# Performance work log

Hardware: AMD Instinct MI355X
Metric: run time of the kernel (lower is better)

## Reference

```python
import jax, jax.numpy as jnp
import numpy as np

B, DIM, HEADS, HD, H, W = 1, 256, 8, 32, 64, 64
MLP = int(DIM * 4.0)
EPS = 1e-5


def _ln(x, g, b):
    # LayerNorm over channel dim of NCHW (torch applies it on NHWC last dim)
    mu = x.mean(axis=1, keepdims=True)
    var = ((x - mu) ** 2).mean(axis=1, keepdims=True)
    return (x - mu) / jnp.sqrt(var + EPS) * g[None, :, None, None] + b[None, :, None, None]


def _c1(x, w, b):
    # 1x1 conv: w is [out, in]
    return jnp.einsum('bchw,oc->bohw', x, w) + b[None, :, None, None]


def _c3(x, w, b):
    y = jax.lax.conv_general_dilated(x, w, (1, 1), ((1, 1), (1, 1)),
                                     dimension_numbers=('NCHW', 'OIHW', 'NCHW'))
    return y + b[None, :, None, None]


def setup_inputs() -> dict:
    key = jax.random.key(0)
    ks = jax.random.split(key, 16)
    init = lambda k, s: jax.random.normal(k, s, jnp.float32) * 0.02
    d = {}
    d['rgb_feat'] = jax.random.normal(ks[0], (B, DIM, H, W), jnp.float32)
    d['dpt_feat'] = jax.random.normal(ks[1], (B, DIM, H, W), jnp.float32)
    d['x_dpt'] = jax.random.normal(ks[2], (B, 1, 1024, 1024), jnp.float32)
    d['wq'] = init(ks[3], (DIM, DIM)); d['bq'] = jnp.zeros((DIM,), jnp.float32)
    d['wk'] = init(ks[4], (DIM, DIM)); d['bk'] = jnp.zeros((DIM,), jnp.float32)
    d['wv'] = init(ks[5], (DIM, DIM)); d['bv'] = jnp.zeros((DIM,), jnp.float32)
    d['wo'] = init(ks[6], (DIM, DIM)); d['bo'] = jnp.zeros((DIM,), jnp.float32)
    d['g_rgb'] = jnp.ones((DIM,), jnp.float32); d['b_rgb'] = jnp.zeros((DIM,), jnp.float32)
    d['g_dpt'] = jnp.ones((DIM,), jnp.float32); d['b_dpt'] = jnp.zeros((DIM,), jnp.float32)
    d['g1'] = jnp.ones((DIM,), jnp.float32); d['b1'] = jnp.zeros((DIM,), jnp.float32)
    d['g2'] = jnp.ones((DIM,), jnp.float32); d['b2'] = jnp.zeros((DIM,), jnp.float32)
    d['w_mlp1'] = init(ks[7], (MLP, DIM)); d['b_mlp1'] = jnp.zeros((MLP,), jnp.float32)
    d['w_mlp2'] = init(ks[8], (DIM, MLP)); d['b_mlp2'] = jnp.zeros((DIM,), jnp.float32)
    d['w_de1'] = init(ks[9], (DIM, 1, 3, 3)); d['b_de1'] = jnp.zeros((DIM,), jnp.float32)
    d['w_de2'] = init(ks[10], (DIM, DIM)); d['b_de2'] = jnp.zeros((DIM,), jnp.float32)
    d['pos_emb'] = init(ks[11], (1, DIM, 1, 1))
    d['scale'] = jnp.sqrt(jnp.float32(HD))
    return d


def reference(rgb_feat, dpt_feat, x_dpt, wq, bq, wk, bk, wv, bv, wo, bo,
              g_rgb, b_rgb, g_dpt, b_dpt, g1, b1, g2, b2,
              w_mlp1, b_mlp1, w_mlp2, b_mlp2, w_de1, b_de1, w_de2, b_de2,
              pos_emb, scale):
    Bn, C, Hh, Ww = rgb_feat.shape
    n = Hh * Ww
    rgb_ln = _ln(rgb_feat, g_rgb, b_rgb)
    dpt_ln = _ln(dpt_feat, g_dpt, b_dpt)
    # depth positional embedding: bilinear downsample (align_corners=False) + conv3x3 + relu + conv1x1
    xd = jax.image.resize(x_dpt, (Bn, 1, Hh, Ww), method='bilinear', antialias=False)
    pe = _c1(jax.nn.relu(_c3(xd, w_de1, b_de1)), w_de2, b_de2)
    rgb_ln = rgb_ln + pos_emb + pe
    dpt_ln = dpt_ln + pos_emb + pe
    # QKV as [B, heads, head_dim, N]
    q = _c1(rgb_ln, wq, bq).reshape(Bn, HEADS, HD, n)
    k = _c1(dpt_ln, wk, bk).reshape(Bn, HEADS, HD, n)
    v = _c1(dpt_ln, wv, bv).reshape(Bn, HEADS, HD, n)
    scores = jnp.einsum('bhdn,bhdm->bhnm', q, k) / scale
    attn = jax.nn.softmax(scores, axis=-1)  # dropout is identity in eval
    fused = jnp.einsum('bhnm,bhdm->bhdn', attn, v).reshape(Bn, C, Hh, Ww)
    out = _c1(fused, wo, bo) + rgb_feat
    out_ln = _ln(out, g1, b1)
    h = jax.nn.gelu(_c1(out_ln, w_mlp1, b_mlp1), approximate=False)
    mlp_out = _c1(h, w_mlp2, b_mlp2)
    out2 = mlp_out + out_ln
    return _ln(out2, g2, b2)
```

## Files before the change

kernel.cpp:

```cpp
#include <hip/hip_runtime.h>
#include <hip/hip_bf16.h>
#include <math.h>

constexpr int NTOK = 4096;
constexpr int CDIM = 256;
constexpr int MLPD = 1024;
constexpr int SPLIT = 4;
constexpr float EPS_LN = 1e-5f;

typedef __attribute__((ext_vector_type(8))) short bf16x8;
typedef __attribute__((ext_vector_type(4))) float floatx4;
typedef unsigned short u16;
typedef unsigned int u32;

__device__ __forceinline__ u16 f2bf(float x) {
    union { float f; u32 u; } v; v.f = x;
    u32 r = v.u + 0x7fff + ((v.u >> 16) & 1);
    return (u16)(r >> 16);
}
__device__ __forceinline__ float bf2f(u16 u) {
    union { u32 i; float f; } v; v.i = ((u32)u) << 16; return v.f;
}
__device__ __forceinline__ u32 pkbf(float a, float b) {
    __hip_bfloat162 h = __float22bfloat162_rn(make_float2(a, b));
    union { __hip_bfloat162 h; u32 u; } v; v.h = h; return v.u;
}
__device__ __forceinline__ float gelu_exact(float x) {
    return 0.5f * x * (1.0f + erff(x * 0.70710678118654752f));
}

__global__ __launch_bounds__(256) void k_tr2(const float* __restrict__ in0,
                                             float* __restrict__ out0,
                                             const float* __restrict__ in1,
                                             float* __restrict__ out1, int R, int C) {
    const float* in = blockIdx.z ? in1 : in0;
    float* out = blockIdx.z ? out1 : out0;
    __shared__ float T[64][65];
    int r0 = blockIdx.y * 64, c0 = blockIdx.x * 64;
    int t = threadIdx.x;
    int rr = t >> 4, cc = (t & 15) * 4;
#pragma unroll
    for (int i = 0; i < 4; ++i) {
        int row = i * 16 + rr;
        float4 v = *(const float4*)(in + (size_t)(r0 + row) * C + c0 + cc);
        T[row][cc] = v.x; T[row][cc + 1] = v.y; T[row][cc + 2] = v.z; T[row][cc + 3] = v.w;
    }
    __syncthreads();
#pragma unroll
    for (int i = 0; i < 4; ++i) {
        int a = i * 16 + rr;
        float4 v;
        v.x = T[cc][a]; v.y = T[cc + 1][a]; v.z = T[cc + 2][a]; v.w = T[cc + 3][a];
        *(float4*)(out + (size_t)(c0 + a) * R + r0 + cc) = v;
    }
}

__global__ __launch_bounds__(256) void k_prep(const float* __restrict__ xdpt,
                                              const float* __restrict__ w3,
                                              const float* __restrict__ b3,
                                              u16* __restrict__ y,
                                              const float* __restrict__ wq,
                                              const float* __restrict__ wk,
                                              const float* __restrict__ wv,
                                              const float* __restrict__ wo,
                                              const float* __restrict__ wde2,
                                              const float* __restrict__ wm1,
                                              const float* __restrict__ wm2,
                                              u16* __restrict__ arena) {
    int blk = blockIdx.x;
    int t = threadIdx.x;
    if (blk < 256) {
        __shared__ float nb[3][18];
        int n0 = blk * 16;
        int yy = n0 >> 6, x0 = n0 & 63;
        if (t < 54) {
            int r = t / 18, cc = t % 18;
            int sy = yy - 1 + r, sx = x0 - 1 + cc;
            float v = 0.f;
            if (sy >= 0 && sy < 64 && sx >= 0 && sx < 64) {
                int r0 = 16 * sy + 7, c0 = 16 * sx + 7;
                v = 0.25f * (xdpt[r0 * 1024 + c0] + xdpt[r0 * 1024 + c0 + 1] +
                             xdpt[(r0 + 1) * 1024 + c0] + xdpt[(r0 + 1) * 1024 + c0 + 1]);
            }
            nb[r][cc] = v;
        }
        __syncthreads();
        float wv9[9];
#pragma unroll
        for (int i = 0; i < 9; ++i) wv9[i] = w3[t * 9 + i];
        float bb = b3[t];
#pragma unroll
        for (int k = 0; k < 16; ++k) {
            float acc = bb;
#pragma unroll
            for (int r = 0; r < 3; ++r)
#pragma unroll
                for (int kx = 0; kx < 3; ++kx) acc += wv9[r * 3 + kx] * nb[r][k + kx];
            y[(size_t)(n0 + k) * CDIM + t] = f2bf(fmaxf(acc, 0.f));
        }
    } else {
        int e0 = (blk - 256) * 1024 + t * 4;
        const float* src; int off;
        if (e0 < 65536)       { src = wq;   off = 0; }
        else if (e0 < 131072) { src = wk;   off = 65536; }
        else if (e0 < 196608) { src = wv;   off = 131072; }
        else if (e0 < 262144) { src = wo;   off = 196608; }
        else if (e0 < 327680) { src = wde2; off = 262144; }
        else if (e0 < 589824) { src = wm1;  off = 327680; }
        else                  { src = wm2;  off = 589824; }
        float4 v = *(const float4*)(src + (e0 - off));
        uint2 o; o.x = pkbf(v.x, v.y); o.y = pkbf(v.z, v.w);
        *(uint2*)(arena + e0) = o;
    }
}

__global__ __launch_bounds__(256) void k_lnT(const void* __restrict__ xA,
                                             const float* __restrict__ gA,
                                             const float* __restrict__ bA,
                                             void* __restrict__ yA,
                                             const void* __restrict__ xB,
                                             const float* __restrict__ gB,
                                             const float* __restrict__ bB,
                                             void* __restrict__ yB,
                                             const u16* __restrict__ pe,
                                             const float* __restrict__ pos,
                                             int xf32, int yf32) {
    const void* x; const float* g; const float* bb; void* y;
    if (blockIdx.y == 0) { x = xA; g = gA; bb = bA; y = yA; }
    else                 { x = xB; g = gB; bb = bB; y = yB; }
    int n = blockIdx.x * 4 + (threadIdx.x >> 6);
    int lane = threadIdx.x & 63;
    int c = lane * 4;
    float4 xv;
    if (xf32) {
        xv = *((const float4*)x + (size_t)n * 64 + lane);
    } else {
        ushort4 u = *((const ushort4*)x + (size_t)n * 64 + lane);
        xv = make_float4(bf2f(u.x), bf2f(u.y), bf2f(u.z), bf2f(u.w));
    }
    float s = xv.x + xv.y + xv.z + xv.w;
    float s2 = xv.x * xv.x + xv.y * xv.y + xv.z * xv.z + xv.w * xv.w;
#pragma unroll
    for (int off = 1; off < 64; off <<= 1) {
        s += __shfl_xor(s, off, 64);
        s2 += __shfl_xor(s2, off, 64);
    }
    float mu = s * (1.0f / 256.0f);
    float var = s2 * (1.0f / 256.0f) - mu * mu;
    float rsd = rsqrtf(var + EPS_LN);
    float4 g4 = *(const float4*)(g + c);
    float4 b4 = *(const float4*)(bb + c);
    float4 o;
    o.x = (xv.x - mu) * rsd * g4.x + b4.x;
    o.y = (xv.y - mu) * rsd * g4.y + b4.y;
    o.z = (xv.z - mu) * rsd * g4.z + b4.z;
    o.w = (xv.w - mu) * rsd * g4.w + b4.w;
    if (pe) {
        float4 p4 = *(const float4*)(pos + c);
        ushort4 pu = *((const ushort4*)pe + (size_t)n * 64 + lane);
        o.x += p4.x + bf2f(pu.x);
        o.y += p4.y + bf2f(pu.y);
        o.z += p4.z + bf2f(pu.z);
        o.w += p4.w + bf2f(pu.w);
    }
    if (yf32) {
        *((float4*)y + (size_t)n * 64 + lane) = o;
    } else {
        ushort4 ou;
        ou.x = f2bf(o.x); ou.y = f2bf(o.y); ou.z = f2bf(o.z); ou.w = f2bf(o.w);
        *((ushort4*)y + (size_t)n * 64 + lane) = ou;
    }
}

#define LDB 72
__global__ __launch_bounds__(256) void k_bmm(const u16* __restrict__ X0, const void* __restrict__ W0,
                                             const float* __restrict__ B0, void* __restrict__ Y0, int f0,
                                             const u16* __restrict__ X1, const void* __restrict__ W1,
                                             const float* __restrict__ B1, void* __restrict__ Y1, int f1,
                                             const u16* __restrict__ X2, const void* __restrict__ W2,
                                             const float* __restrict__ B2, void* __restrict__ Y2, int f2,
                                             const void* __restrict__ res, const float* __restrict__ scl,
                                             int M, int K) {
    const u16* X; const void* Wp; const float* bias; void* Yp; int flags;
    if (blockIdx.z == 0)      { X = X0; Wp = W0; bias = B0; Yp = Y0; flags = f0; }
    else if (blockIdx.z == 1) { X = X1; Wp = W1; bias = B1; Yp = Y1; flags = f1; }
    else                      { X = X2; Wp = W2; bias = B2; Yp = Y2; flags = f2; }
    __shared__ u16 Xs[64 * LDB];
    __shared__ u16 Ws[64 * LDB];
    int tid = threadIdx.x;
    int wid = tid >> 6, lane = tid & 63;
    int lo16 = lane & 15, quad = lane >> 4;
    int wy = wid & 1, wx = wid >> 1;
    int n0 = blockIdx.x * 64, m0 = blockIdx.y * 64;
    int srow = tid >> 2, sseg = tid & 3;

    floatx4 acc[2][2];
#pragma unroll
    for (int i = 0; i < 2; ++i)
#pragma unroll
        for (int j = 0; j < 2; ++j) acc[i][j] = floatx4{0.f, 0.f, 0.f, 0.f};

    for (int k0 = 0; k0 < K; k0 += 64) {
        const u16* xp = X + (size_t)(n0 + srow) * K + k0 + sseg * 16;
        uint4 xr0 = *(const uint4*)xp;
        uint4 xr1 = *(const uint4*)(xp + 8);
        uint4 wb0, wb1;
        if (flags & 32) {
            const u16* wp = (const u16*)Wp + (size_t)(m0 + srow) * K + k0 + sseg * 16;
            wb0 = *(const uint4*)wp;
            wb1 = *(const uint4*)(wp + 8);
        } else {
            const float* wp = (const float*)Wp + (size_t)(m0 + srow) * K + k0 + sseg * 16;
            float4 w0 = *(const float4*)wp;
            float4 w1 = *(const float4*)(wp + 4);
            float4 w2 = *(const float4*)(wp + 8);
            float4 w3 = *(const float4*)(wp + 12);
            wb0.x = pkbf(w0.x, w0.y); wb0.y = pkbf(w0.z, w0.w);
            wb0.z = pkbf(w1.x, w1.y); wb0.w = pkbf(w1.z, w1.w);
            wb1.x = pkbf(w2.x, w2.y); wb1.y = pkbf(w2.z, w2.w);
            wb1.z = pkbf(w3.x, w3.y); wb1.w = pkbf(w3.z, w3.w);
        }
        if (k0) __syncthreads();
        *(uint4*)&Xs[srow * LDB + sseg * 16] = xr0;
        *(uint4*)&Xs[srow * LDB + sseg * 16 + 8] = xr1;
        *(uint4*)&Ws[srow * LDB + sseg * 16] = wb0;
        *(uint4*)&Ws[srow * LDB + sseg * 16 + 8] = wb1;
        __syncthreads();

        const u16* As = (flags & 2) ? Ws : Xs;
        const u16* Bs = (flags & 2) ? Xs : Ws;
#pragma unroll
        for (int h = 0; h < 2; ++h) {
            int ko = h * 32 + quad * 8;
            bf16x8 a0 = *(const bf16x8*)&As[(wy * 32 + lo16) * LDB + ko];
            bf16x8 a1 = *(const bf16x8*)&As[(wy * 32 + 16 + lo16) * LDB + ko];
            bf16x8 b0 = *(const bf16x8*)&Bs[(wx * 32 + lo16) * LDB + ko];
            bf16x8 b1 = *(const bf16x8*)&Bs[(wx * 32 + 16 + lo16) * LDB + ko];
            acc[0][0] = __builtin_amdgcn_mfma_f32_16x16x32_bf16(a0, b0, acc[0][0], 0, 0, 0);
            acc[0][1] = __builtin_amdgcn_mfma_f32_16x16x32_bf16(a0, b1, acc[0][1], 0, 0, 0);
            acc[1][0] = __builtin_amdgcn_mfma_f32_16x16x32_bf16(a1, b0, acc[1][0], 0, 0, 0);
            acc[1][1] = __builtin_amdgcn_mfma_f32_16x16x32_bf16(a1, b1, acc[1][1], 0, 0, 0);
        }
    }

    u16* Y = (u16*)Yp;
    if (flags & 2) {
#pragma unroll
        for (int i = 0; i < 2; ++i)
#pragma unroll
            for (int r = 0; r < 4; ++r) {
                int ch = m0 + wy * 32 + i * 16 + quad * 4 + r;
                float bb = bias[ch];
#pragma unroll
                for (int j = 0; j < 2; ++j) {
                    int tok = n0 + wx * 32 + j * 16 + lo16;
                    Y[(size_t)ch * NTOK + tok] = f2bf(acc[i][j][r] + bb);
                }
            }
    } else {
        float smul = (flags & 16) ? 1.4426950408889634f / scl[0] : 1.0f;
        float bj0 = bias[m0 + wx * 32 + lo16];
        float bj1 = bias[m0 + wx * 32 + 16 + lo16];
        const float* rf = (const float*)res;
        const u16* rb = (const u16*)res;
#pragma unroll
        for (int i = 0; i < 2; ++i)
#pragma unroll
            for (int j = 0; j < 2; ++j) {
                int ch = m0 + wx * 32 + j * 16 + lo16;
                float bb = j ? bj1 : bj0;
#pragma unroll
                for (int r = 0; r < 4; ++r) {
                    int tok = n0 + wy * 32 + i * 16 + quad * 4 + r;
                    float v = (acc[i][j][r] + bb) * smul;
                    if (flags & 1) v = gelu_exact(v);
                    if (flags & 4) v += rf[(size_t)tok * M + ch];
                    if (flags & 8) v += bf2f(rb[(size_t)tok * M + ch]);
                    if (flags & 64)
                        Y[((size_t)(ch >> 5) * NTOK + tok) * 32 + (ch & 31)] = f2bf(v);
                    else
                        Y[(size_t)tok * M + ch] = f2bf(v);
                }
            }
    }
}

#define LDK 40
#define LDV 72
__global__ __launch_bounds__(256, 8) void k_fattn(const u16* __restrict__ Qh,
                                                  const u16* __restrict__ Kh,
                                                  const u16* __restrict__ Vc,
                                                  u16* __restrict__ Op,
                                                  float* __restrict__ Lp) {
    int h = blockIdx.y;
    int q0 = blockIdx.x * 64;
    int sp = blockIdx.z;
    int tid = threadIdx.x;
    int wid = tid >> 6, lane = tid & 63;
    int lo16 = lane & 15, quad = lane >> 4;

    __shared__ u16 Kt[64 * LDK];
    __shared__ u16 Vt[32 * LDV];
    __shared__ u16 Pt[4][16 * LDV];

    bf16x8 aq = *(const bf16x8*)(Qh + ((size_t)h * NTOK + q0 + wid * 16 + lo16) * 32 + quad * 8);

    floatx4 o0 = {0.f, 0.f, 0.f, 0.f};
    floatx4 o1 = {0.f, 0.f, 0.f, 0.f};
    float l = 0.f;

    int krow = tid >> 2, kseg = tid & 3;
    int vrow = tid >> 3, vseg = tid & 7;
    int kbase = sp * (NTOK / SPLIT);

    for (int kt = 0; kt < NTOK / SPLIT / 64; ++kt) {
        int k0 = kbase + kt * 64;
        uint4 kreg = *(const uint4*)(Kh + ((size_t)h * NTOK + k0 + krow) * 32 + kseg * 8);
        uint4 vreg = *(const uint4*)(Vc + (size_t)(h * 32 + vrow) * NTOK + k0 + vseg * 8);
        __syncthreads();
        *(uint4*)&Kt[krow * LDK + kseg * 8] = kreg;
        *(uint4*)&Vt[vrow * LDV + vseg * 8] = vreg;
        __syncthreads();

        floatx4 s[4];
        floatx4 z = {0.f, 0.f, 0.f, 0.f};
#pragma unroll
        for (int c = 0; c < 4; ++c) {
            bf16x8 ak = *(const bf16x8*)&Kt[(c * 16 + lo16) * LDK + quad * 8];
            s[c] = __builtin_amdgcn_mfma_f32_16x16x32_bf16(ak, aq, z, 0, 0, 0);
        }
        float rs = 0.f;
#pragma unroll
        for (int c = 0; c < 4; ++c)
#pragma unroll
            for (int r = 0; r < 4; ++r) {
                float p = __builtin_amdgcn_exp2f(s[c][r]);
                s[c][r] = p;
                rs += p;
            }
        rs += __shfl_xor(rs, 16, 64);
        rs += __shfl_xor(rs, 32, 64);
        l += rs;
#pragma unroll
        for (int c = 0; c < 4; ++c) {
            uint2 w;
            w.x = pkbf(s[c][0], s[c][1]);
            w.y = pkbf(s[c][2], s[c][3]);
            *(uint2*)&Pt[wid][lo16 * LDV + c * 16 + quad * 4] = w;
        }
#pragma unroll
        for (int kc = 0; kc < 2; ++kc) {
            bf16x8 bp = *(const bf16x8*)&Pt[wid][lo16 * LDV + kc * 32 + quad * 8];
            bf16x8 av0 = *(const bf16x8*)&Vt[lo16 * LDV + kc * 32 + quad * 8];
            bf16x8 av1 = *(const bf16x8*)&Vt[(16 + lo16) * LDV + kc * 32 + quad * 8];
            o0 = __builtin_amdgcn_mfma_f32_16x16x32_bf16(av0, bp, o0, 0, 0, 0);
            o1 = __builtin_amdgcn_mfma_f32_16x16x32_bf16(av1, bp, o1, 0, 0, 0);
        }
    }

    size_t tok = q0 + wid * 16 + lo16;
    size_t obase = ((size_t)(sp * 8 + h) * NTOK + tok) * 32;
    uint2 w0; w0.x = pkbf(o0[0], o0[1]); w0.y = pkbf(o0[2], o0[3]);
    *(uint2*)(Op + obase + quad * 4) = w0;
    uint2 w1; w1.x = pkbf(o1[0], o1[1]); w1.y = pkbf(o1[2], o1[3]);
    *(uint2*)(Op + obase + 16 + quad * 4) = w1;
    if (lane < 16) Lp[(size_t)(sp * 8 + h) * NTOK + tok] = l;
}

__global__ __launch_bounds__(256) void k_comb(const u16* __restrict__ Op,
                                              const float* __restrict__ Lp,
                                              u16* __restrict__ fused) {
    int n = blockIdx.x * 4 + (threadIdx.x >> 6);
    int lane = threadIdx.x & 63;
    int c = lane * 4;
    int h = c >> 5, d = c & 31;
    float4 o = {0.f, 0.f, 0.f, 0.f};
    float l = 0.f;
#pragma unroll
    for (int s = 0; s < SPLIT; ++s) {
        size_t base = ((size_t)(s * 8 + h) * NTOK + n) * 32 + d;
        uint2 u = *(const uint2*)(Op + base);
        o.x += bf2f((u16)(u.x & 0xffff)); o.y += bf2f((u16)(u.x >> 16));
        o.z += bf2f((u16)(u.y & 0xffff)); o.w += bf2f((u16)(u.y >> 16));
        l += Lp[(size_t)(s * 8 + h) * NTOK + n];
    }
    float inv = 1.0f / l;
    uint2 w;
    w.x = pkbf(o.x * inv, o.y * inv);
    w.y = pkbf(o.z * inv, o.w * inv);
    *(uint2*)(fused + (size_t)n * CDIM + c) = w;
}

extern "C" void kernel_launch(void* const* d_in, const int* in_sizes, int n_in,
                              void* d_out, int out_size, void* d_ws, size_t ws_size,
                              hipStream_t stream) {
    const float* rgb    = (const float*)d_in[0];
    const float* dpt    = (const float*)d_in[1];
    const float* x_dpt  = (const float*)d_in[2];
    const float* wq     = (const float*)d_in[3];
    const float* bq     = (const float*)d_in[4];
    const float* wk     = (const float*)d_in[5];
    const float* bk     = (const float*)d_in[6];
    const float* wv     = (const float*)d_in[7];
    const float* bv     = (const float*)d_in[8];
    const float* wo     = (const float*)d_in[9];
    const float* bo     = (const float*)d_in[10];
    const float* g_rgb  = (const float*)d_in[11];
    const float* b_rgb  = (const float*)d_in[12];
    const float* g_dpt  = (const float*)d_in[13];
    const float* b_dpt  = (const float*)d_in[14];
    const float* g1     = (const float*)d_in[15];
    const float* b1     = (const float*)d_in[16];
    const float* g2     = (const float*)d_in[17];
    const float* b2     = (const float*)d_in[18];
    const float* w_mlp1 = (const float*)d_in[19];
    const float* b_mlp1 = (const float*)d_in[20];
    const float* w_mlp2 = (const float*)d_in[21];
    const float* b_mlp2 = (const float*)d_in[22];
    const float* w_de1  = (const float*)d_in[23];
    const float* b_de1  = (const float*)d_in[24];
    const float* w_de2  = (const float*)d_in[25];
    const float* b_de2  = (const float*)d_in[26];
    const float* pos    = (const float*)d_in[27];
    const float* scale  = (const float*)d_in[28];
    float* out = (float*)d_out;

    char* base = (char*)d_ws;
    const size_t MB = 1u << 20;
    float* rgbT    = (float*)(base + 0 * MB);
    float* dptT    = (float*)(base + 4 * MB);
    u16*   outT    = (u16*)(base + 4 * MB);
    float* Lp      = (float*)(base + 6 * MB);
    u16*   out_lnT = (u16*)(base + 6 * MB);
    u16*   relu3T  = (u16*)(base + 8 * MB);
    u16*   peT     = (u16*)(base + 10 * MB);
    u16*   Op      = (u16*)(base + 8 * MB);
    u16*   hT      = (u16*)(base + 8 * MB);
    u16*   aqT     = (u16*)(base + 12 * MB);
    u16*   akvT    = (u16*)(base + 14 * MB);
    u16*   Qhm     = (u16*)(base + 16 * MB);
    u16*   Khm     = (u16*)(base + 18 * MB);
    u16*   out2T   = (u16*)(base + 16 * MB);
    u16*   Vcm     = (u16*)(base + 20 * MB);
    u16*   fusedT  = (u16*)(base + 22 * MB);
    float* lnoutT  = (float*)(base + 20 * MB);
    u16*   arena   = (u16*)(base + 24 * MB);

    bool aw = ws_size >= 26 * MB;
    int wf = aw ? 32 : 0;
    const void* Wq  = aw ? (const void*)(arena + 0)      : (const void*)wq;
    const void* Wk  = aw ? (const void*)(arena + 65536)  : (const void*)wk;
    const void* Wv  = aw ? (const void*)(arena + 131072) : (const void*)wv;
    const void* Wo  = aw ? (const void*)(arena + 196608) : (const void*)wo;
    const void* Wd2 = aw ? (const void*)(arena + 262144) : (const void*)w_de2;
    const void* Wm1 = aw ? (const void*)(arena + 327680) : (const void*)w_mlp1;
    const void* Wm2 = aw ? (const void*)(arena + 589824) : (const void*)w_mlp2;

    k_tr2<<<dim3(NTOK / 64, CDIM / 64, 2), 256, 0, stream>>>(rgb, rgbT, dpt, dptT, CDIM, NTOK);
    k_prep<<<aw ? 256 + 832 : 256, 256, 0, stream>>>(x_dpt, w_de1, b_de1, relu3T,
                                                     wq, wk, wv, wo, w_de2, w_mlp1, w_mlp2, arena);
    k_bmm<<<dim3(64, 4, 1), 256, 0, stream>>>(relu3T, Wd2, b_de2, peT, wf,
                                              nullptr, nullptr, nullptr, nullptr, 0,
                                              nullptr, nullptr, nullptr, nullptr, 0,
                                              nullptr, nullptr, CDIM, CDIM);
    k_lnT<<<dim3(1024, 2), 256, 0, stream>>>(rgbT, g_rgb, b_rgb, aqT,
                                             dptT, g_dpt, b_dpt, akvT,
                                             peT, pos, 1, 0);
    k_bmm<<<dim3(64, 4, 3), 256, 0, stream>>>(aqT, Wq, bq, Qhm, wf | 16 | 64,
                                              akvT, Wk, bk, Khm, wf | 64,
                                              akvT, Wv, bv, Vcm, wf | 2,
                                              nullptr, scale, CDIM, CDIM);
    k_fattn<<<dim3(64, 8, SPLIT), 256, 0, stream>>>(Qhm, Khm, Vcm, Op, Lp);
    k_comb<<<1024, 256, 0, stream>>>(Op, Lp, fusedT);
    k_bmm<<<dim3(64, 4, 1), 256, 0, stream>>>(fusedT, Wo, bo, outT, wf | 4,
                                              nullptr, nullptr, nullptr, nullptr, 0,
                                              nullptr, nullptr, nullptr, nullptr, 0,
                                              rgbT, nullptr, CDIM, CDIM);
    k_lnT<<<dim3(1024, 1), 256, 0, stream>>>(outT, g1, b1, out_lnT,
                                             nullptr, nullptr, nullptr, nullptr,
                                             nullptr, nullptr, 0, 0);
    k_bmm<<<dim3(64, 16, 1), 256, 0, stream>>>(out_lnT, Wm1, b_mlp1, hT, wf | 1,
                                               nullptr, nullptr, nullptr, nullptr, 0,
                                               nullptr, nullptr, nullptr, nullptr, 0,
                                               nullptr, nullptr, MLPD, CDIM);
    k_bmm<<<dim3(64, 4, 1), 256, 0, stream>>>(hT, Wm2, b_mlp2, out2T, wf | 8,
                                              nullptr, nullptr, nullptr, nullptr, 0,
                                              nullptr, nullptr, nullptr, nullptr, 0,
                                              out_lnT, nullptr, CDIM, MLPD);
    k_lnT<<<dim3(1024, 1), 256, 0, stream>>>(out2T, g2, b2, lnoutT,
                                             nullptr, nullptr, nullptr, nullptr,
                                             nullptr, nullptr, 0, 1);
    k_tr2<<<dim3(CDIM / 64, NTOK / 64, 1), 256, 0, stream>>>(lnoutT, out, nullptr, nullptr, NTOK, CDIM);
}
```

Before: 226.9 us.

## Fuse input transpose into prep, fuse final LN with transpose, rework attention loads

Folds the input NCHW→NHWC transpose into the prep kernel and merges the final LayerNorm with the output transpose into one kernel, removing two launches and an fp32 intermediate round trip. The flash-attention kernel stops staging K and V through shared memory with block barriers. Each wave now reads K and V fragments straight from global memory and stores P in a swizzled per-wave buffer, with launch bounds lowered to 4 waves per SIMD. This drops synchronisation and LDS traffic, but each wave now issues its own redundant global loads of K/V, and occupancy may be lower.

```diff
diff --git a/kernel.cpp b/kernel.cpp
--- a/kernel.cpp
+++ b/kernel.cpp
@@ -29,33 +29,11 @@
     return 0.5f * x * (1.0f + erff(x * 0.70710678118654752f));
 }
 
-__global__ __launch_bounds__(256) void k_tr2(const float* __restrict__ in0,
-                                             float* __restrict__ out0,
-                                             const float* __restrict__ in1,
-                                             float* __restrict__ out1, int R, int C) {
-    const float* in = blockIdx.z ? in1 : in0;
-    float* out = blockIdx.z ? out1 : out0;
-    __shared__ float T[64][65];
-    int r0 = blockIdx.y * 64, c0 = blockIdx.x * 64;
-    int t = threadIdx.x;
-    int rr = t >> 4, cc = (t & 15) * 4;
-#pragma unroll
-    for (int i = 0; i < 4; ++i) {
-        int row = i * 16 + rr;
-        float4 v = *(const float4*)(in + (size_t)(r0 + row) * C + c0 + cc);
-        T[row][cc] = v.x; T[row][cc + 1] = v.y; T[row][cc + 2] = v.z; T[row][cc + 3] = v.w;
-    }
-    __syncthreads();
-#pragma unroll
-    for (int i = 0; i < 4; ++i) {
-        int a = i * 16 + rr;
-        float4 v;
-        v.x = T[cc][a]; v.y = T[cc + 1][a]; v.z = T[cc + 2][a]; v.w = T[cc + 3][a];
-        *(float4*)(out + (size_t)(c0 + a) * R + r0 + cc) = v;
-    }
-}
-
-__global__ __launch_bounds__(256) void k_prep(const float* __restrict__ xdpt,
+__global__ __launch_bounds__(256) void k_prep(const float* __restrict__ rgb,
+                                              float* __restrict__ rgbT,
+                                              const float* __restrict__ dpt,
+                                              float* __restrict__ dptT,
+                                              const float* __restrict__ xdpt,
                                               const float* __restrict__ w3,
                                               const float* __restrict__ b3,
                                               u16* __restrict__ y,
@@ -69,9 +47,30 @@
                                               u16* __restrict__ arena) {
     int blk = blockIdx.x;
     int t = threadIdx.x;
-    if (blk < 256) {
+    if (blk < 512) {
+        const float* in = (blk < 256) ? rgb : dpt;
+        float* out = (blk < 256) ? rgbT : dptT;
+        int tb = blk & 255;
+        int c0 = (tb & 63) * 64, r0 = (tb >> 6) * 64;
+        __shared__ float T[64][65];
+        int rr = t >> 4, cc = (t & 15) * 4;
+#pragma unroll
+        for (int i = 0; i < 4; ++i) {
+            int row = i * 16 + rr;
+            float4 v = *(const float4*)(in + (size_t)(r0 + row) * NTOK + c0 + cc);
+            T[row][cc] = v.x; T[row][cc + 1] = v.y; T[row][cc + 2] = v.z; T[row][cc + 3] = v.w;
+        }
+        __syncthreads();
+#pragma unroll
+        for (int i = 0; i < 4; ++i) {
+            int a = i * 16 + rr;
+            float4 v;
+            v.x = T[cc][a]; v.y = T[cc + 1][a]; v.z = T[cc + 2][a]; v.w = T[cc + 3][a];
+            *(float4*)(out + (size_t)(c0 + a) * CDIM + r0 + cc) = v;
+        }
+    } else if (blk < 768) {
         __shared__ float nb[3][18];
-        int n0 = blk * 16;
+        int n0 = (blk - 512) * 16;
         int yy = n0 >> 6, x0 = n0 & 63;
         if (t < 54) {
             int r = t / 18, cc = t % 18;
@@ -99,7 +98,7 @@
             y[(size_t)(n0 + k) * CDIM + t] = f2bf(fmaxf(acc, 0.f));
         }
     } else {
-        int e0 = (blk - 256) * 1024 + t * 4;
+        int e0 = (blk - 768) * 1024 + t * 4;
         const float* src; int off;
         if (e0 < 65536)       { src = wq;   off = 0; }
         else if (e0 < 131072) { src = wk;   off = 65536; }
@@ -124,7 +123,7 @@
                                              void* __restrict__ yB,
                                              const u16* __restrict__ pe,
                                              const float* __restrict__ pos,
-                                             int xf32, int yf32) {
+                                             int xf32) {
     const void* x; const float* g; const float* bb; void* y;
     if (blockIdx.y == 0) { x = xA; g = gA; bb = bA; y = yA; }
     else                 { x = xB; g = gB; bb = bB; y = yB; }
@@ -163,13 +162,9 @@
         o.z += p4.z + bf2f(pu.z);
         o.w += p4.w + bf2f(pu.w);
     }
-    if (yf32) {
-        *((float4*)y + (size_t)n * 64 + lane) = o;
-    } else {
-        ushort4 ou;
-        ou.x = f2bf(o.x); ou.y = f2bf(o.y); ou.z = f2bf(o.z); ou.w = f2bf(o.w);
-        *((ushort4*)y + (size_t)n * 64 + lane) = ou;
-    }
+    ushort4 ou;
+    ou.x = f2bf(o.x); ou.y = f2bf(o.y); ou.z = f2bf(o.z); ou.w = f2bf(o.w);
+    *((ushort4*)y + (size_t)n * 64 + lane) = ou;
 }
 
 #define LDB 72
@@ -285,50 +280,47 @@
     }
 }
 
-#define LDK 40
-#define LDV 72
-__global__ __launch_bounds__(256, 8) void k_fattn(const u16* __restrict__ Qh,
+#define LDP 72
+__global__ __launch_bounds__(256, 4) void k_fattn(const u16* __restrict__ Qh,
                                                   const u16* __restrict__ Kh,
                                                   const u16* __restrict__ Vc,
                                                   u16* __restrict__ Op,
                                                   float* __restrict__ Lp) {
     int h = blockIdx.y;
-    int q0 = blockIdx.x * 64;
     int sp = blockIdx.z;
     int tid = threadIdx.x;
     int wid = tid >> 6, lane = tid & 63;
     int lo16 = lane & 15, quad = lane >> 4;
-
-    __shared__ u16 Kt[64 * LDK];
-    __shared__ u16 Vt[32 * LDV];
-    __shared__ u16 Pt[4][16 * LDV];
-
-    bf16x8 aq = *(const bf16x8*)(Qh + ((size_t)h * NTOK + q0 + wid * 16 + lo16) * 32 + quad * 8);
+    int q0 = blockIdx.x * 64 + wid * 16;
+
+    __shared__ u16 Pt[4][16 * LDP];
+    u16* P = &Pt[wid][0];
+    int swz = (lo16 & 3) * 32;
+    char* prow = (char*)P + lo16 * (LDP * 2);
+
+    bf16x8 aq = *(const bf16x8*)(Qh + ((size_t)h * NTOK + q0 + lo16) * 32 + quad * 8);
+    const u16* kp = Kh + (size_t)h * NTOK * 32;
+    const u16* vp0 = Vc + (size_t)lo16 * NTOK;
+    const u16* vp1 = Vc + (size_t)(16 + lo16) * NTOK;
+    size_t hv = (size_t)h * 32 * NTOK;
 
     floatx4 o0 = {0.f, 0.f, 0.f, 0.f};
     floatx4 o1 = {0.f, 0.f, 0.f, 0.f};
     float l = 0.f;
 
-    int krow = tid >> 2, kseg = tid & 3;
-    int vrow = tid >> 3, vseg = tid & 7;
-    int kbase = sp * (NTOK / SPLIT);
-
     for (int kt = 0; kt < NTOK / SPLIT / 64; ++kt) {
-        int k0 = kbase + kt * 64;
-        uint4 kreg = *(const uint4*)(Kh + ((size_t)h * NTOK + k0 + krow) * 32 + kseg * 8);
-        uint4 vreg = *(const uint4*)(Vc + (size_t)(h * 32 + vrow) * NTOK + k0 + vseg * 8);
-        __syncthreads();
-        *(uint4*)&Kt[krow * LDK + kseg * 8] = kreg;
-        *(uint4*)&Vt[vrow * LDV + vseg * 8] = vreg;
-        __syncthreads();
-
+        int k0 = sp * (NTOK / SPLIT) + kt * 64;
         floatx4 s[4];
         floatx4 z = {0.f, 0.f, 0.f, 0.f};
 #pragma unroll
         for (int c = 0; c < 4; ++c) {
-            bf16x8 ak = *(const bf16x8*)&Kt[(c * 16 + lo16) * LDK + quad * 8];
+            bf16x8 ak = *(const bf16x8*)(kp + (size_t)(k0 + c * 16 + lo16) * 32 + quad * 8);
             s[c] = __builtin_amdgcn_mfma_f32_16x16x32_bf16(ak, aq, z, 0, 0, 0);
         }
+        bf16x8 av00 = *(const bf16x8*)(vp0 + hv + k0 + quad * 8);
+        bf16x8 av10 = *(const bf16x8*)(vp1 + hv + k0 + quad * 8);
+        bf16x8 av01 = *(const bf16x8*)(vp0 + hv + k0 + 32 + quad * 8);
+        bf16x8 av11 = *(const bf16x8*)(vp1 + hv + k0 + 32 + quad * 8);
         float rs = 0.f;
 #pragma unroll
         for (int c = 0; c < 4; ++c)
@@ -346,25 +338,23 @@
             uint2 w;
             w.x = pkbf(s[c][0], s[c][1]);
             w.y = pkbf(s[c][2], s[c][3]);
-            *(uint2*)&Pt[wid][lo16 * LDV + c * 16 + quad * 4] = w;
+            *(uint2*)(prow + ((c * 32 + quad * 8) ^ swz)) = w;
         }
 #pragma unroll
         for (int kc = 0; kc < 2; ++kc) {
-            bf16x8 bp = *(const bf16x8*)&Pt[wid][lo16 * LDV + kc * 32 + quad * 8];
-            bf16x8 av0 = *(const bf16x8*)&Vt[lo16 * LDV + kc * 32 + quad * 8];
-            bf16x8 av1 = *(const bf16x8*)&Vt[(16 + lo16) * LDV + kc * 32 + quad * 8];
-            o0 = __builtin_amdgcn_mfma_f32_16x16x32_bf16(av0, bp, o0, 0, 0, 0);
-            o1 = __builtin_amdgcn_mfma_f32_16x16x32_bf16(av1, bp, o1, 0, 0, 0);
-        }
-    }
-
-    size_t tok = q0 + wid * 16 + lo16;
+            bf16x8 bp = *(const bf16x8*)(prow + ((kc * 64 + quad * 16) ^ swz));
+            o0 = __builtin_amdgcn_mfma_f32_16x16x32_bf16(kc ? av01 : av00, bp, o0, 0, 0, 0);
+            o1 = __builtin_amdgcn_mfma_f32_16x16x32_bf16(kc ? av11 : av10, bp, o1, 0, 0, 0);
+        }
+    }
+
+    size_t tok = q0 + lo16;
     size_t obase = ((size_t)(sp * 8 + h) * NTOK + tok) * 32;
     uint2 w0; w0.x = pkbf(o0[0], o0[1]); w0.y = pkbf(o0[2], o0[3]);
     *(uint2*)(Op + obase + quad * 4) = w0;
     uint2 w1; w1.x = pkbf(o1[0], o1[1]); w1.y = pkbf(o1[2], o1[3]);
     *(uint2*)(Op + obase + 16 + quad * 4) = w1;
-    if (lane < 16) Lp[(size_t)(sp * 8 + h) * NTOK + tok] = l;
+    if (quad == 0) Lp[(size_t)(sp * 8 + h) * NTOK + tok] = l;
 }
 
 __global__ __launch_bounds__(256) void k_comb(const u16* __restrict__ Op,
@@ -389,6 +379,55 @@
     w.x = pkbf(o.x * inv, o.y * inv);
     w.y = pkbf(o.z * inv, o.w * inv);
     *(uint2*)(fused + (size_t)n * CDIM + c) = w;
+}
+
+__global__ __launch_bounds__(256) void k_lntr(const u16* __restrict__ x,
+                                              const float* __restrict__ g,
+                                              const float* __restrict__ b,
+                                              float* __restrict__ out) {
+    __shared__ float T[16][260];
+    int n0 = blockIdx.x * 16;
+    int t = threadIdx.x;
+    int tk = t >> 4, seg = t & 15;
+    float v[16];
+    {
+        const u16* p = x + (size_t)(n0 + tk) * CDIM + seg * 16;
+        uint4 a = *(const uint4*)p;
+        uint4 bq = *(const uint4*)(p + 8);
+        u32 uu[8] = {a.x, a.y, a.z, a.w, bq.x, bq.y, bq.z, bq.w};
+#pragma unroll
+        for (int i = 0; i < 8; ++i) {
+            v[2 * i] = bf2f((u16)(uu[i] & 0xffff));
+            v[2 * i + 1] = bf2f((u16)(uu[i] >> 16));
+        }
+    }
+    float s = 0.f, s2 = 0.f;
+#pragma unroll
+    for (int i = 0; i < 16; ++i) { s += v[i]; s2 += v[i] * v[i]; }
+#pragma unroll
+    for (int off = 1; off < 16; off <<= 1) {
+        s += __shfl_xor(s, off, 64);
+        s2 += __shfl_xor(s2, off, 64);
+    }
+    float mu = s * (1.0f / 256.0f);
+    float var = s2 * (1.0f / 256.0f) - mu * mu;
+    float rsd = rsqrtf(var + EPS_LN);
+#pragma unroll
+    for (int i = 0; i < 16; ++i) {
+        int c = seg * 16 + i;
+        T[tk][c] = (v[i] - mu) * rsd * g[c] + b[c];
+    }
+    __syncthreads();
+    int c = t;
+    float o[16];
+#pragma unroll
+    for (int j = 0; j < 16; ++j) o[j] = T[j][c];
+    float* dst = out + (size_t)c * NTOK + n0;
+#pragma unroll
+    for (int j = 0; j < 4; ++j) {
+        float4 w = {o[4 * j], o[4 * j + 1], o[4 * j + 2], o[4 * j + 3]};
+        *(float4*)(dst + 4 * j) = w;
+    }
 }
 
 extern "C" void kernel_launch(void* const* d_in, const int* in_sizes, int n_in,
@@ -443,7 +482,6 @@
     u16*   out2T   = (u16*)(base + 16 * MB);
     u16*   Vcm     = (u16*)(base + 20 * MB);
     u16*   fusedT  = (u16*)(base + 22 * MB);
-    float* lnoutT  = (float*)(base + 20 * MB);
     u16*   arena   = (u16*)(base + 24 * MB);
 
     bool aw = ws_size >= 26 * MB;
@@ -456,16 +494,16 @@
     const void* Wm1 = aw ? (const void*)(arena + 327680) : (const void*)w_mlp1;
     const void* Wm2 = aw ? (const void*)(arena + 589824) : (const void*)w_mlp2;
 
-    k_tr2<<<dim3(NTOK / 64, CDIM / 64, 2), 256, 0, stream>>>(rgb, rgbT, dpt, dptT, CDIM, NTOK);
-    k_prep<<<aw ? 256 + 832 : 256, 256, 0, stream>>>(x_dpt, w_de1, b_de1, relu3T,
-                                                     wq, wk, wv, wo, w_de2, w_mlp1, w_mlp2, arena);
+    k_prep<<<aw ? 512 + 256 + 832 : 512 + 256, 256, 0, stream>>>(
+        rgb, rgbT, dpt, dptT, x_dpt, w_de1, b_de1, relu3T,
+        wq, wk, wv, wo, w_de2, w_mlp1, w_mlp2, arena);
     k_bmm<<<dim3(64, 4, 1), 256, 0, stream>>>(relu3T, Wd2, b_de2, peT, wf,
                                               nullptr, nullptr, nullptr, nullptr, 0,
                                               nullptr, nullptr, nullptr, nullptr, 0,
                                               nullptr, nullptr, CDIM, CDIM);
     k_lnT<<<dim3(1024, 2), 256, 0, stream>>>(rgbT, g_rgb, b_rgb, aqT,
                                              dptT, g_dpt, b_dpt, akvT,
-                                             peT, pos, 1, 0);
+                                             peT, pos, 1);
     k_bmm<<<dim3(64, 4, 3), 256, 0, stream>>>(aqT, Wq, bq, Qhm, wf | 16 | 64,
                                               akvT, Wk, bk, Khm, wf | 64,
                                               akvT, Wv, bv, Vcm, wf | 2,
@@ -478,7 +516,7 @@
                                               rgbT, nullptr, CDIM, CDIM);
     k_lnT<<<dim3(1024, 1), 256, 0, stream>>>(outT, g1, b1, out_lnT,
                                              nullptr, nullptr, nullptr, nullptr,
-                                             nullptr, nullptr, 0, 0);
+                                             nullptr, nullptr, 0);
     k_bmm<<<dim3(64, 16, 1), 256, 0, stream>>>(out_lnT, Wm1, b_mlp1, hT, wf | 1,
                                                nullptr, nullptr, nullptr, nullptr, 0,
                                                nullptr, nullptr, nullptr, nullptr, 0,
@@ -487,8 +525,5 @@
                                               nullptr, nullptr, nullptr, nullptr, 0,
                                               nullptr, nullptr, nullptr, nullptr, 0,
                                               out_lnT, nullptr, CDIM, MLPD);
-    k_lnT<<<dim3(1024, 1), 256, 0, stream>>>(out2T, g2, b2, lnoutT,
-                                             nullptr, nullptr, nullptr, nullptr,
-                                             nullptr, nullptr, 0, 1);
-    k_tr2<<<dim3(CDIM / 64, NTOK / 64, 1), 256, 0, stream>>>(lnoutT, out, nullptr, nullptr, NTOK, CDIM);
-}
+    k_lntr<<<256, 256, 0, stream>>>(out2T, g2, b2, out);
+}
```

New measurement: 270.0 us. 1.19x slower.
